# Kernel tuning notes

Hardware: AMD Instinct MI355X
Metric: run time of the kernel (lower is better)

Reference implementation:

```python
import jax, jax.numpy as jnp
import numpy as np

N = 1024      # number of nodes
D = 128       # d_x
H = 8         # num_heads


def setup_inputs() -> dict:
    key = jax.random.key(0)
    ks = jax.random.split(key, 7)
    s = (D * H) ** -0.5
    return {
        "x": jax.random.normal(ks[0], (N, D), dtype=jnp.float32),
        "spatial_encoding": jax.random.normal(ks[1], (N, N), dtype=jnp.float32),
        "edge_encoding": jax.random.normal(ks[2], (N, N), dtype=jnp.float32),
        "Wq": jax.random.normal(ks[3], (D * H, D), dtype=jnp.float32) * s,
        "Wk": jax.random.normal(ks[4], (D * H, D), dtype=jnp.float32) * s,
        "Wv": jax.random.normal(ks[5], (D * H, D), dtype=jnp.float32) * s,
        "Wo": jax.random.normal(ks[6], (D, D * H), dtype=jnp.float32) * s,
    }


def reference(x, spatial_encoding, edge_encoding, Wq, Wk, Wv, Wo):
    n, d = x.shape
    h = Wq.shape[0] // d
    scale = d ** -0.5
    # Linear (no bias), then the module's peculiar view: [n, d*h] -> [d, n, h]
    q = (x @ Wq.T).reshape(d, n, h)            # [d, n, h]
    k = (x @ Wk.T).reshape(d, n, h)            # [d, n, h]
    v = (x @ Wv.T).reshape(d, n, h)            # [d, n, h]
    # a = q @ k^T over head dim: [d, n, n]
    a = jnp.einsum('dnh,dmh->dnm', q, k) * scale
    a = a + spatial_encoding + edge_encoding   # [n,n] biases broadcast over d
    a = jax.nn.softmax(a, axis=2)
    # dropout is identity at inference
    out = jnp.einsum('dnm,dmh->dnh', a, v)     # [d, n, h]
    out = out.reshape(n, h * d)                # row-major reshape, same as torch
    return out @ Wo.T                          # [n, d]
```

## Files before the change

kernel.cpp:

```cpp
#include <hip/hip_runtime.h>
#include <hip/hip_bf16.h>
#include <math.h>

#define N_NODES 1024
#define D_DIM   128
#define H_HEADS 8
#define DH      1024

typedef short  short8 __attribute__((ext_vector_type(8)));
typedef float  f32x16 __attribute__((ext_vector_type(16)));
typedef unsigned short us4 __attribute__((ext_vector_type(4)));

static __device__ __forceinline__ unsigned short f2bf(float x) {
    __hip_bfloat16 h = __float2bfloat16(x);
    return *reinterpret_cast<unsigned short*>(&h);
}
static __device__ __forceinline__ unsigned cvt_pk_bf16(float lo, float hi) {
    unsigned r;
    asm volatile("v_cvt_pk_bf16_f32 %0, %1, %2" : "=v"(r) : "v"(lo), "v"(hi));
    return r;
}
static __device__ __forceinline__ void permlane32_swap(unsigned &a, unsigned &b) {
    asm volatile("v_permlane32_swap_b32 %0, %1" : "+v"(a), "+v"(b));
}
static __device__ __forceinline__ float fast_exp2(float x) {
    float r;
    asm("v_exp_f32 %0, %1" : "=v"(r) : "v"(x));
    return r;
}

__global__ __launch_bounds__(256) void bias_q_kernel(const float* __restrict__ sp,
                                                     const float* __restrict__ ed,
                                                     float* __restrict__ Bq) {
    __shared__ float tile[32][33];
    const int cb = blockIdx.x, rb = blockIdx.y, tid = threadIdx.x;
    const float L2E = 1.4426950408889634f;
    for (int i = tid; i < 1024; i += 256) {
        int rr = i >> 5, cc = i & 31;
        size_t g = (size_t)(rb * 32 + rr) * 1024 + cb * 32 + cc;
        tile[rr][cc] = (sp[g] + ed[g]) * L2E;
    }
    __syncthreads();
    const int c4l = tid >> 5, rr = tid & 31;
    float4 v = make_float4(tile[rr][4 * c4l + 0], tile[rr][4 * c4l + 1],
                           tile[rr][4 * c4l + 2], tile[rr][4 * c4l + 3]);
    reinterpret_cast<float4*>(Bq)[(size_t)(cb * 8 + c4l) * 1024 + rb * 32 + rr] = v;
}

__global__ __launch_bounds__(256) void qkv_mfma_kernel(const float* __restrict__ x,
                                                       const float* __restrict__ Wq,
                                                       const float* __restrict__ Wk,
                                                       const float* __restrict__ Wv,
                                                       unsigned short* __restrict__ Q,
                                                       unsigned short* __restrict__ K,
                                                       unsigned short* __restrict__ V) {
    const int tid = threadIdx.x, lane = tid & 63, wvi = tid >> 6;
    const int l31 = lane & 31, hi = lane >> 5;
    const int rb0 = blockIdx.x * 128 + wvi * 32;
    const int col = blockIdx.y * 32 + l31;
    const int m   = blockIdx.z;
    const float* W        = (m == 0) ? Wq : (m == 1) ? Wk : Wv;
    unsigned short* Out   = (m == 0) ? Q  : (m == 1) ? K  : V;
    const float osc = (m == 0) ? 0.12751879523173864f : 1.0f;

    const float* xrow = x + (size_t)(rb0 + l31) * 128 + 8 * hi;
    const float* wrow = W + (size_t)col * 128 + 8 * hi;

    f32x16 acc = {};
    #pragma unroll
    for (int ks = 0; ks < 8; ++ks) {
        float4 xa = *reinterpret_cast<const float4*>(xrow + ks * 16);
        float4 xb = *reinterpret_cast<const float4*>(xrow + ks * 16 + 4);
        float4 wa = *reinterpret_cast<const float4*>(wrow + ks * 16);
        float4 wb = *reinterpret_cast<const float4*>(wrow + ks * 16 + 4);
        union { short8 s8; unsigned u[4]; } af, bf;
        af.u[0] = cvt_pk_bf16(xa.x, xa.y); af.u[1] = cvt_pk_bf16(xa.z, xa.w);
        af.u[2] = cvt_pk_bf16(xb.x, xb.y); af.u[3] = cvt_pk_bf16(xb.z, xb.w);
        bf.u[0] = cvt_pk_bf16(wa.x, wa.y); bf.u[1] = cvt_pk_bf16(wa.z, wa.w);
        bf.u[2] = cvt_pk_bf16(wb.x, wb.y); bf.u[3] = cvt_pk_bf16(wb.z, wb.w);
        acc = __builtin_amdgcn_mfma_f32_32x32x16_bf16(af.s8, bf.s8, acc, 0, 0, 0);
    }
    #pragma unroll
    for (int i = 0; i < 16; ++i) {
        int mm = (i & 3) + 8 * (i >> 2) + 4 * hi;
        Out[(size_t)(rb0 + mm) * DH + col] = f2bf(acc[i] * osc);
    }
}

__global__ __launch_bounds__(256) void attn_kernel(const unsigned short* __restrict__ Qb,
                                                   const unsigned short* __restrict__ Kb,
                                                   const unsigned short* __restrict__ Vb,
                                                   const float* __restrict__ Bq,
                                                   unsigned short* __restrict__ Oh,
                                                   unsigned short* __restrict__ Ol) {
    __shared__ unsigned short Vt[9216];
    const int dd  = blockIdx.y;
    const int tid = threadIdx.x, lane = tid & 63, wvi = tid >> 6;
    const int l31 = lane & 31, hi = lane >> 5;

    {
        const unsigned short* src = Vb + (size_t)dd * 8192;
        char* base = reinterpret_cast<char*>(Vt);
        #pragma unroll
        for (int it = 0; it < 2; ++it) {
            int pr = it * 256 + tid;
            short8 v0 = *reinterpret_cast<const short8*>(src + (size_t)(2 * pr) * 8);
            short8 v1 = *reinterpret_cast<const short8*>(src + (size_t)(2 * pr + 1) * 8);
            #pragma unroll
            for (int h = 0; h < 8; ++h) {
                unsigned d = (unsigned)(unsigned short)v0[h] |
                             ((unsigned)(unsigned short)v1[h] << 16);
                *reinterpret_cast<unsigned*>(base + h * 2048 + ((4 * pr) ^ (h << 4))) = d;
            }
        }
        reinterpret_cast<unsigned*>(base + 16384)[tid]       = 0x3F803F80u;
        reinterpret_cast<unsigned*>(base + 16384)[tid + 256] = 0x3F803F80u;
    }
    __syncthreads();

    const int r = blockIdx.x * 128 + wvi * 32 + l31;
    short8 qf = {};
    if (!hi) qf = *reinterpret_cast<const short8*>(Qb + (size_t)dd * 8192 + (size_t)r * 8);

    f32x16 oacc = {};
    const unsigned short* kp = Kb + (size_t)dd * 8192 + (size_t)l31 * 8;
    const float4* bq4 = reinterpret_cast<const float4*>(Bq) + (size_t)hi * 1024 + r;

    auto load_bias = [&](int cbv) -> f32x16 {
        const float4* b = bq4 + (size_t)cbv * 8192;
        float4 b0 = b[0], b1 = b[2048], b2 = b[4096], b3 = b[6144];
        f32x16 o;
        o[0] = b0.x; o[1] = b0.y; o[2]  = b0.z; o[3]  = b0.w;
        o[4] = b1.x; o[5] = b1.y; o[6]  = b1.z; o[7]  = b1.w;
        o[8] = b2.x; o[9] = b2.y; o[10] = b2.z; o[11] = b2.w;
        o[12] = b3.x; o[13] = b3.y; o[14] = b3.z; o[15] = b3.w;
        return o;
    };
    auto load_k = [&](int cbv) -> short8 {
        return *reinterpret_cast<const short8*>(kp + (size_t)cbv * 256);
    };
    auto step = [&](int cbv, const f32x16& bias, const short8& kfv) {
        f32x16 sf = bias;
        sf = __builtin_amdgcn_mfma_f32_32x32x16_bf16(kfv, qf, sf, 0, 0, 0);
        float p[16];
        #pragma unroll
        for (int i = 0; i < 16; ++i) p[i] = fast_exp2(sf[i]);
        unsigned u0 = cvt_pk_bf16(p[0],  p[1]);
        unsigned u1 = cvt_pk_bf16(p[2],  p[3]);
        unsigned u2 = cvt_pk_bf16(p[4],  p[5]);
        unsigned u3 = cvt_pk_bf16(p[6],  p[7]);
        unsigned u4 = cvt_pk_bf16(p[8],  p[9]);
        unsigned u5 = cvt_pk_bf16(p[10], p[11]);
        unsigned u6 = cvt_pk_bf16(p[12], p[13]);
        unsigned u7 = cvt_pk_bf16(p[14], p[15]);
        permlane32_swap(u0, u2);
        permlane32_swap(u1, u3);
        permlane32_swap(u4, u6);
        permlane32_swap(u5, u7);
        union { short8 s8; unsigned u[4]; } pb1, pb2;
        pb1.u[0] = u0; pb1.u[1] = u1; pb1.u[2] = u2; pb1.u[3] = u3;
        pb2.u[0] = u4; pb2.u[1] = u5; pb2.u[2] = u6; pb2.u[3] = u7;

        short8 vf1 = {}, vf2 = {};
        if (l31 < 9) {
            const char* vb = reinterpret_cast<const char*>(Vt) + l31 * 2048;
            vf1 = *reinterpret_cast<const short8*>(vb + ((cbv * 64 + 16 * hi)      ^ (l31 << 4)));
            vf2 = *reinterpret_cast<const short8*>(vb + ((cbv * 64 + 32 + 16 * hi) ^ (l31 << 4)));
        }
        oacc = __builtin_amdgcn_mfma_f32_32x32x16_bf16(vf1, pb1.s8, oacc, 0, 0, 0);
        oacc = __builtin_amdgcn_mfma_f32_32x32x16_bf16(vf2, pb2.s8, oacc, 0, 0, 0);
    };

    f32x16 bA = load_bias(0), bB = load_bias(1);
    short8 kA = load_k(0),   kB = load_k(1);
    for (int cb = 0; cb < 32; cb += 2) {
        step(cb, bA, kA);
        if (cb < 30) { bA = load_bias(cb + 2); kA = load_k(cb + 2); }
        step(cb + 1, bB, kB);
        if (cb < 30) { bB = load_bias(cb + 3); kB = load_k(cb + 3); }
    }

    const float ls = oacc[4] + __shfl_xor(oacc[4], 32, 64);
    const float rl = 1.f / ls;
    us4 h4, l4;
    #pragma unroll
    for (int i = 0; i < 4; ++i) {
        float v = oacc[i] * rl;
        unsigned uv = __float_as_uint(v);
        h4[i] = (unsigned short)(uv >> 16);
        l4[i] = f2bf(v - __uint_as_float(uv & 0xFFFF0000u));
    }
    size_t off = (size_t)dd * 8192 + (size_t)r * 8 + 4 * hi;
    *reinterpret_cast<us4*>(Oh + off) = h4;
    *reinterpret_cast<us4*>(Ol + off) = l4;
}

__global__ __launch_bounds__(256) void oproj_kernel(const unsigned short* __restrict__ Oh,
                                                    const unsigned short* __restrict__ Ol,
                                                    const float* __restrict__ Wo,
                                                    float* __restrict__ out) {
    __shared__ float red[4][1024];
    const int tid = threadIdx.x, lane = tid & 63, wvi = tid >> 6;
    const int l31 = lane & 31, hi = lane >> 5;
    const int rbase = blockIdx.x * 32, cbase = blockIdx.y * 32;

    const unsigned short* ah_p = Oh + (size_t)(rbase + l31) * 1024 + wvi * 256 + 8 * hi;
    const unsigned short* al_p = Ol + (size_t)(rbase + l31) * 1024 + wvi * 256 + 8 * hi;
    const float*          b_p  = Wo + (size_t)(cbase + l31) * 1024 + wvi * 256 + 8 * hi;

    f32x16 acc = {};
    #pragma unroll
    for (int ks = 0; ks < 16; ++ks) {
        short8 ah = *reinterpret_cast<const short8*>(ah_p + ks * 16);
        short8 al = *reinterpret_cast<const short8*>(al_p + ks * 16);
        float4 w0 = *reinterpret_cast<const float4*>(b_p + ks * 16);
        float4 w1 = *reinterpret_cast<const float4*>(b_p + ks * 16 + 4);
        float w[8] = { w0.x, w0.y, w0.z, w0.w, w1.x, w1.y, w1.z, w1.w };
        union { short8 s8; unsigned u[4]; } bh, bl;
        float lo[8];
        #pragma unroll
        for (int j = 0; j < 8; ++j) {
            unsigned uv = __float_as_uint(w[j]);
            lo[j] = w[j] - __uint_as_float(uv & 0xFFFF0000u);
        }
        #pragma unroll
        for (int j = 0; j < 4; ++j) {
            unsigned e = __float_as_uint(w[2 * j]) >> 16;
            unsigned o = __float_as_uint(w[2 * j + 1]) & 0xFFFF0000u;
            bh.u[j] = e | o;
            bl.u[j] = cvt_pk_bf16(lo[2 * j], lo[2 * j + 1]);
        }
        acc = __builtin_amdgcn_mfma_f32_32x32x16_bf16(ah, bh.s8, acc, 0, 0, 0);
        acc = __builtin_amdgcn_mfma_f32_32x32x16_bf16(al, bh.s8, acc, 0, 0, 0);
        acc = __builtin_amdgcn_mfma_f32_32x32x16_bf16(ah, bl.s8, acc, 0, 0, 0);
    }
    #pragma unroll
    for (int i = 0; i < 16; ++i) {
        int mm = (i & 3) + 8 * (i >> 2) + 4 * hi;
        red[wvi][mm * 32 + l31] = acc[i];
    }
    __syncthreads();
    #pragma unroll
    for (int t = 0; t < 4; ++t) {
        int idx = tid + t * 256;
        float v = red[0][idx] + red[1][idx] + red[2][idx] + red[3][idx];
        out[(size_t)(rbase + (idx >> 5)) * D_DIM + cbase + (idx & 31)] = v;
    }
}

extern "C" void kernel_launch(void* const* d_in, const int* in_sizes, int n_in,
                              void* d_out, int out_size, void* d_ws, size_t ws_size,
                              hipStream_t stream) {
    const float* x  = (const float*)d_in[0];
    const float* sp = (const float*)d_in[1];
    const float* ed = (const float*)d_in[2];
    const float* Wq = (const float*)d_in[3];
    const float* Wk = (const float*)d_in[4];
    const float* Wv = (const float*)d_in[5];
    const float* Wo = (const float*)d_in[6];
    float* out = (float*)d_out;

    float* ws = (float*)d_ws;
    const size_t M = (size_t)N_NODES * DH;
    float* Bq = ws;
    unsigned short* Qb = (unsigned short*)(ws + M);
    unsigned short* Kb = Qb + M;
    unsigned short* Vb = Kb + M;
    unsigned short* Oh = Vb + M;
    unsigned short* Ol = Oh + M;

    bias_q_kernel<<<dim3(32, 32), 256, 0, stream>>>(sp, ed, Bq);
    qkv_mfma_kernel<<<dim3(8, 32, 3), 256, 0, stream>>>(x, Wq, Wk, Wv, Qb, Kb, Vb);
    attn_kernel<<<dim3(8, 128), 256, 0, stream>>>(Qb, Kb, Vb, Bq, Oh, Ol);
    oproj_kernel<<<dim3(32, 4), 256, 0, stream>>>(Oh, Ol, Wo, out);
}
```

Before: 68.07 us.

## Split attention keys across two chunks, merge QKV/bias prep, shrink oproj tiles

Attention now splits the key dimension into two halves, each handled by its own block, and writes unnormalized partial outputs and row sums. A new combine kernel adds the halves, normalizes, and splits the result into bf16 hi/lo. The QKV projection and bias kernels are merged into one launch. The output projection moves to 16x16 MFMA tiles to launch more blocks. The aim is more blocks and parallelism per launch; the cost is an extra kernel launch and extra fp32 partial-result traffic through memory.

New measurement: 66.42 us. 2.4% less time.

```diff
diff --git a/kernel.cpp b/kernel.cpp
--- a/kernel.cpp
+++ b/kernel.cpp
@@ -9,6 +9,7 @@
 
 typedef short  short8 __attribute__((ext_vector_type(8)));
 typedef float  f32x16 __attribute__((ext_vector_type(16)));
+typedef float  f32x4  __attribute__((ext_vector_type(4)));
 typedef unsigned short us4 __attribute__((ext_vector_type(4)));
 
 static __device__ __forceinline__ unsigned short f2bf(float x) {
@@ -29,61 +30,67 @@
     return r;
 }
 
-__global__ __launch_bounds__(256) void bias_q_kernel(const float* __restrict__ sp,
-                                                     const float* __restrict__ ed,
-                                                     float* __restrict__ Bq) {
+__global__ __launch_bounds__(256) void prep_kernel(const float* __restrict__ x,
+                                                   const float* __restrict__ Wq,
+                                                   const float* __restrict__ Wk,
+                                                   const float* __restrict__ Wv,
+                                                   const float* __restrict__ sp,
+                                                   const float* __restrict__ ed,
+                                                   unsigned short* __restrict__ Q,
+                                                   unsigned short* __restrict__ K,
+                                                   unsigned short* __restrict__ V,
+                                                   float* __restrict__ Bq) {
     __shared__ float tile[32][33];
-    const int cb = blockIdx.x, rb = blockIdx.y, tid = threadIdx.x;
-    const float L2E = 1.4426950408889634f;
-    for (int i = tid; i < 1024; i += 256) {
-        int rr = i >> 5, cc = i & 31;
-        size_t g = (size_t)(rb * 32 + rr) * 1024 + cb * 32 + cc;
-        tile[rr][cc] = (sp[g] + ed[g]) * L2E;
-    }
-    __syncthreads();
-    const int c4l = tid >> 5, rr = tid & 31;
-    float4 v = make_float4(tile[rr][4 * c4l + 0], tile[rr][4 * c4l + 1],
-                           tile[rr][4 * c4l + 2], tile[rr][4 * c4l + 3]);
-    reinterpret_cast<float4*>(Bq)[(size_t)(cb * 8 + c4l) * 1024 + rb * 32 + rr] = v;
-}
-
-__global__ __launch_bounds__(256) void qkv_mfma_kernel(const float* __restrict__ x,
-                                                       const float* __restrict__ Wq,
-                                                       const float* __restrict__ Wk,
-                                                       const float* __restrict__ Wv,
-                                                       unsigned short* __restrict__ Q,
-                                                       unsigned short* __restrict__ K,
-                                                       unsigned short* __restrict__ V) {
-    const int tid = threadIdx.x, lane = tid & 63, wvi = tid >> 6;
-    const int l31 = lane & 31, hi = lane >> 5;
-    const int rb0 = blockIdx.x * 128 + wvi * 32;
-    const int col = blockIdx.y * 32 + l31;
-    const int m   = blockIdx.z;
-    const float* W        = (m == 0) ? Wq : (m == 1) ? Wk : Wv;
-    unsigned short* Out   = (m == 0) ? Q  : (m == 1) ? K  : V;
-    const float osc = (m == 0) ? 0.12751879523173864f : 1.0f;
-
-    const float* xrow = x + (size_t)(rb0 + l31) * 128 + 8 * hi;
-    const float* wrow = W + (size_t)col * 128 + 8 * hi;
-
-    f32x16 acc = {};
-    #pragma unroll
-    for (int ks = 0; ks < 8; ++ks) {
-        float4 xa = *reinterpret_cast<const float4*>(xrow + ks * 16);
-        float4 xb = *reinterpret_cast<const float4*>(xrow + ks * 16 + 4);
-        float4 wa = *reinterpret_cast<const float4*>(wrow + ks * 16);
-        float4 wb = *reinterpret_cast<const float4*>(wrow + ks * 16 + 4);
-        union { short8 s8; unsigned u[4]; } af, bf;
-        af.u[0] = cvt_pk_bf16(xa.x, xa.y); af.u[1] = cvt_pk_bf16(xa.z, xa.w);
-        af.u[2] = cvt_pk_bf16(xb.x, xb.y); af.u[3] = cvt_pk_bf16(xb.z, xb.w);
-        bf.u[0] = cvt_pk_bf16(wa.x, wa.y); bf.u[1] = cvt_pk_bf16(wa.z, wa.w);
-        bf.u[2] = cvt_pk_bf16(wb.x, wb.y); bf.u[3] = cvt_pk_bf16(wb.z, wb.w);
-        acc = __builtin_amdgcn_mfma_f32_32x32x16_bf16(af.s8, bf.s8, acc, 0, 0, 0);
-    }
-    #pragma unroll
-    for (int i = 0; i < 16; ++i) {
-        int mm = (i & 3) + 8 * (i >> 2) + 4 * hi;
-        Out[(size_t)(rb0 + mm) * DH + col] = f2bf(acc[i] * osc);
+    const int bid = blockIdx.x;
+    const int tid = threadIdx.x;
+
+    if (bid < 768) {
+        const int lane = tid & 63, wvi = tid >> 6;
+        const int l31 = lane & 31, hi = lane >> 5;
+        const int m   = bid >> 8;
+        const int rem = bid & 255;
+        const int rb0 = (rem & 7) * 128 + wvi * 32;
+        const int col = (rem >> 3) * 32 + l31;
+        const float* W        = (m == 0) ? Wq : (m == 1) ? Wk : Wv;
+        unsigned short* Out   = (m == 0) ? Q  : (m == 1) ? K  : V;
+        const float osc = (m == 0) ? 0.12751879523173864f : 1.0f;
+
+        const float* xrow = x + (size_t)(rb0 + l31) * 128 + 8 * hi;
+        const float* wrow = W + (size_t)col * 128 + 8 * hi;
+
+        f32x16 acc = {};
+        #pragma unroll
+        for (int ks = 0; ks < 8; ++ks) {
+            float4 xa = *reinterpret_cast<const float4*>(xrow + ks * 16);
+            float4 xb = *reinterpret_cast<const float4*>(xrow + ks * 16 + 4);
+            float4 wa = *reinterpret_cast<const float4*>(wrow + ks * 16);
+            float4 wb = *reinterpret_cast<const float4*>(wrow + ks * 16 + 4);
+            union { short8 s8; unsigned u[4]; } af, bf;
+            af.u[0] = cvt_pk_bf16(xa.x, xa.y); af.u[1] = cvt_pk_bf16(xa.z, xa.w);
+            af.u[2] = cvt_pk_bf16(xb.x, xb.y); af.u[3] = cvt_pk_bf16(xb.z, xb.w);
+            bf.u[0] = cvt_pk_bf16(wa.x, wa.y); bf.u[1] = cvt_pk_bf16(wa.z, wa.w);
+            bf.u[2] = cvt_pk_bf16(wb.x, wb.y); bf.u[3] = cvt_pk_bf16(wb.z, wb.w);
+            acc = __builtin_amdgcn_mfma_f32_32x32x16_bf16(af.s8, bf.s8, acc, 0, 0, 0);
+        }
+        #pragma unroll
+        for (int i = 0; i < 16; ++i) {
+            int mm = (i & 3) + 8 * (i >> 2) + 4 * hi;
+            Out[(size_t)(rb0 + mm) * DH + col] = f2bf(acc[i] * osc);
+        }
+    } else {
+        const int b2 = bid - 768;
+        const int cb = b2 & 31, rb = b2 >> 5;
+        const float L2E = 1.4426950408889634f;
+        for (int i = tid; i < 1024; i += 256) {
+            int rr = i >> 5, cc = i & 31;
+            size_t g = (size_t)(rb * 32 + rr) * 1024 + cb * 32 + cc;
+            tile[rr][cc] = (sp[g] + ed[g]) * L2E;
+        }
+        __syncthreads();
+        const int c4l = tid >> 5, rr = tid & 31;
+        float4 v = make_float4(tile[rr][4 * c4l + 0], tile[rr][4 * c4l + 1],
+                               tile[rr][4 * c4l + 2], tile[rr][4 * c4l + 3]);
+        reinterpret_cast<float4*>(Bq)[(size_t)(cb * 8 + c4l) * 1024 + rb * 32 + rr] = v;
     }
 }
 
@@ -91,30 +98,26 @@
                                                    const unsigned short* __restrict__ Kb,
                                                    const unsigned short* __restrict__ Vb,
                                                    const float* __restrict__ Bq,
-                                                   unsigned short* __restrict__ Oh,
-                                                   unsigned short* __restrict__ Ol) {
-    __shared__ unsigned short Vt[9216];
-    const int dd  = blockIdx.y;
+                                                   float* __restrict__ Opart,
+                                                   float* __restrict__ Lpart) {
+    __shared__ unsigned short Vt[9 * 512];
+    const int dd = blockIdx.y, ch = blockIdx.z;
     const int tid = threadIdx.x, lane = tid & 63, wvi = tid >> 6;
     const int l31 = lane & 31, hi = lane >> 5;
 
     {
-        const unsigned short* src = Vb + (size_t)dd * 8192;
+        const unsigned short* src = Vb + (size_t)dd * 8192 + (size_t)ch * 4096;
         char* base = reinterpret_cast<char*>(Vt);
-        #pragma unroll
-        for (int it = 0; it < 2; ++it) {
-            int pr = it * 256 + tid;
-            short8 v0 = *reinterpret_cast<const short8*>(src + (size_t)(2 * pr) * 8);
-            short8 v1 = *reinterpret_cast<const short8*>(src + (size_t)(2 * pr + 1) * 8);
-            #pragma unroll
-            for (int h = 0; h < 8; ++h) {
-                unsigned d = (unsigned)(unsigned short)v0[h] |
-                             ((unsigned)(unsigned short)v1[h] << 16);
-                *reinterpret_cast<unsigned*>(base + h * 2048 + ((4 * pr) ^ (h << 4))) = d;
-            }
-        }
-        reinterpret_cast<unsigned*>(base + 16384)[tid]       = 0x3F803F80u;
-        reinterpret_cast<unsigned*>(base + 16384)[tid + 256] = 0x3F803F80u;
+        int pr = tid;
+        short8 v0 = *reinterpret_cast<const short8*>(src + (size_t)(2 * pr) * 8);
+        short8 v1 = *reinterpret_cast<const short8*>(src + (size_t)(2 * pr + 1) * 8);
+        #pragma unroll
+        for (int h = 0; h < 8; ++h) {
+            unsigned d = (unsigned)(unsigned short)v0[h] |
+                         ((unsigned)(unsigned short)v1[h] << 16);
+            *reinterpret_cast<unsigned*>(base + h * 1024 + ((4 * pr) ^ (h << 4))) = d;
+        }
+        reinterpret_cast<unsigned*>(base + 8 * 1024)[tid] = 0x3F803F80u;
     }
     __syncthreads();
 
@@ -123,8 +126,9 @@
     if (!hi) qf = *reinterpret_cast<const short8*>(Qb + (size_t)dd * 8192 + (size_t)r * 8);
 
     f32x16 oacc = {};
-    const unsigned short* kp = Kb + (size_t)dd * 8192 + (size_t)l31 * 8;
-    const float4* bq4 = reinterpret_cast<const float4*>(Bq) + (size_t)hi * 1024 + r;
+    const unsigned short* kp = Kb + (size_t)dd * 8192 + (size_t)(ch * 512 + l31) * 8;
+    const float4* bq4 = reinterpret_cast<const float4*>(Bq)
+                        + (size_t)ch * 131072 + (size_t)hi * 1024 + r;
 
     auto load_bias = [&](int cbv) -> f32x16 {
         const float4* b = bq4 + (size_t)cbv * 8192;
@@ -163,7 +167,7 @@
 
         short8 vf1 = {}, vf2 = {};
         if (l31 < 9) {
-            const char* vb = reinterpret_cast<const char*>(Vt) + l31 * 2048;
+            const char* vb = reinterpret_cast<const char*>(Vt) + l31 * 1024;
             vf1 = *reinterpret_cast<const short8*>(vb + ((cbv * 64 + 16 * hi)      ^ (l31 << 4)));
             vf2 = *reinterpret_cast<const short8*>(vb + ((cbv * 64 + 32 + 16 * hi) ^ (l31 << 4)));
         }
@@ -173,79 +177,84 @@
 
     f32x16 bA = load_bias(0), bB = load_bias(1);
     short8 kA = load_k(0),   kB = load_k(1);
-    for (int cb = 0; cb < 32; cb += 2) {
+    for (int cb = 0; cb < 16; cb += 2) {
         step(cb, bA, kA);
-        if (cb < 30) { bA = load_bias(cb + 2); kA = load_k(cb + 2); }
+        if (cb < 14) { bA = load_bias(cb + 2); kA = load_k(cb + 2); }
         step(cb + 1, bB, kB);
-        if (cb < 30) { bB = load_bias(cb + 3); kB = load_k(cb + 3); }
-    }
-
-    const float ls = oacc[4] + __shfl_xor(oacc[4], 32, 64);
-    const float rl = 1.f / ls;
-    us4 h4, l4;
+        if (cb < 14) { bB = load_bias(cb + 3); kB = load_k(cb + 3); }
+    }
+
+    size_t off = (size_t)ch * 1048576 + (size_t)dd * 8192 + (size_t)r * 8 + 4 * hi;
+    *reinterpret_cast<float4*>(Opart + off) =
+        make_float4(oacc[0], oacc[1], oacc[2], oacc[3]);
+    if (!hi) Lpart[(size_t)ch * 131072 + (size_t)dd * 1024 + r] = oacc[4];
+}
+
+__global__ __launch_bounds__(256) void combine_kernel(const float* __restrict__ Opart,
+                                                      const float* __restrict__ Lpart,
+                                                      unsigned short* __restrict__ Oh,
+                                                      unsigned short* __restrict__ Ol) {
+    const int gid = blockIdx.x * 256 + threadIdx.x;
+    const float4* p1 = reinterpret_cast<const float4*>(Opart) + (size_t)gid * 2;
+    const float4* p2 = reinterpret_cast<const float4*>(Opart + 1048576) + (size_t)gid * 2;
+    float4 a0 = p1[0], a1 = p1[1], b0 = p2[0], b1 = p2[1];
+    const float rl = 1.f / (Lpart[gid] + Lpart[131072 + gid]);
+    float v[8] = { (a0.x + b0.x) * rl, (a0.y + b0.y) * rl,
+                   (a0.z + b0.z) * rl, (a0.w + b0.w) * rl,
+                   (a1.x + b1.x) * rl, (a1.y + b1.y) * rl,
+                   (a1.z + b1.z) * rl, (a1.w + b1.w) * rl };
+    union { short8 s8; unsigned short us[8]; } h8, l8;
     #pragma unroll
-    for (int i = 0; i < 4; ++i) {
-        float v = oacc[i] * rl;
-        unsigned uv = __float_as_uint(v);
-        h4[i] = (unsigned short)(uv >> 16);
-        l4[i] = f2bf(v - __uint_as_float(uv & 0xFFFF0000u));
-    }
-    size_t off = (size_t)dd * 8192 + (size_t)r * 8 + 4 * hi;
-    *reinterpret_cast<us4*>(Oh + off) = h4;
-    *reinterpret_cast<us4*>(Ol + off) = l4;
+    for (int i = 0; i < 8; ++i) {
+        unsigned uv = __float_as_uint(v[i]);
+        h8.us[i] = (unsigned short)(uv >> 16);
+        l8.us[i] = f2bf(v[i] - __uint_as_float(uv & 0xFFFF0000u));
+    }
+    *reinterpret_cast<short8*>(Oh + (size_t)gid * 8) = h8.s8;
+    *reinterpret_cast<short8*>(Ol + (size_t)gid * 8) = l8.s8;
 }
 
 __global__ __launch_bounds__(256) void oproj_kernel(const unsigned short* __restrict__ Oh,
                                                     const unsigned short* __restrict__ Ol,
                                                     const float* __restrict__ Wo,
                                                     float* __restrict__ out) {
-    __shared__ float red[4][1024];
+    __shared__ float red[4][256];
     const int tid = threadIdx.x, lane = tid & 63, wvi = tid >> 6;
-    const int l31 = lane & 31, hi = lane >> 5;
-    const int rbase = blockIdx.x * 32, cbase = blockIdx.y * 32;
-
-    const unsigned short* ah_p = Oh + (size_t)(rbase + l31) * 1024 + wvi * 256 + 8 * hi;
-    const unsigned short* al_p = Ol + (size_t)(rbase + l31) * 1024 + wvi * 256 + 8 * hi;
-    const float*          b_p  = Wo + (size_t)(cbase + l31) * 1024 + wvi * 256 + 8 * hi;
-
-    f32x16 acc = {};
+    const int l15 = lane & 15, kg = lane >> 4;
+    const int rbase = blockIdx.x * 16, cbase = blockIdx.y * 16;
+
+    const unsigned short* ah_p = Oh + (size_t)(rbase + l15) * 1024 + wvi * 256 + kg * 8;
+    const unsigned short* al_p = Ol + (size_t)(rbase + l15) * 1024 + wvi * 256 + kg * 8;
+    const float*          b_p  = Wo + (size_t)(cbase + l15) * 1024 + wvi * 256 + kg * 8;
+
+    f32x4 acc = {};
     #pragma unroll
-    for (int ks = 0; ks < 16; ++ks) {
-        short8 ah = *reinterpret_cast<const short8*>(ah_p + ks * 16);
-        short8 al = *reinterpret_cast<const short8*>(al_p + ks * 16);
-        float4 w0 = *reinterpret_cast<const float4*>(b_p + ks * 16);
-        float4 w1 = *reinterpret_cast<const float4*>(b_p + ks * 16 + 4);
+    for (int ks = 0; ks < 8; ++ks) {
+        short8 ah = *reinterpret_cast<const short8*>(ah_p + ks * 32);
+        short8 al = *reinterpret_cast<const short8*>(al_p + ks * 32);
+        float4 w0 = *reinterpret_cast<const float4*>(b_p + ks * 32);
+        float4 w1 = *reinterpret_cast<const float4*>(b_p + ks * 32 + 4);
         float w[8] = { w0.x, w0.y, w0.z, w0.w, w1.x, w1.y, w1.z, w1.w };
         union { short8 s8; unsigned u[4]; } bh, bl;
-        float lo[8];
-        #pragma unroll
-        for (int j = 0; j < 8; ++j) {
-            unsigned uv = __float_as_uint(w[j]);
-            lo[j] = w[j] - __uint_as_float(uv & 0xFFFF0000u);
-        }
         #pragma unroll
         for (int j = 0; j < 4; ++j) {
             unsigned e = __float_as_uint(w[2 * j]) >> 16;
             unsigned o = __float_as_uint(w[2 * j + 1]) & 0xFFFF0000u;
             bh.u[j] = e | o;
-            bl.u[j] = cvt_pk_bf16(lo[2 * j], lo[2 * j + 1]);
-        }
-        acc = __builtin_amdgcn_mfma_f32_32x32x16_bf16(ah, bh.s8, acc, 0, 0, 0);
-        acc = __builtin_amdgcn_mfma_f32_32x32x16_bf16(al, bh.s8, acc, 0, 0, 0);
-        acc = __builtin_amdgcn_mfma_f32_32x32x16_bf16(ah, bl.s8, acc, 0, 0, 0);
+            float lo0 = w[2 * j]     - __uint_as_float(__float_as_uint(w[2 * j])     & 0xFFFF0000u);
+            float lo1 = w[2 * j + 1] - __uint_as_float(__float_as_uint(w[2 * j + 1]) & 0xFFFF0000u);
+            bl.u[j] = cvt_pk_bf16(lo0, lo1);
+        }
+        acc = __builtin_amdgcn_mfma_f32_16x16x32_bf16(ah, bh.s8, acc, 0, 0, 0);
+        acc = __builtin_amdgcn_mfma_f32_16x16x32_bf16(al, bh.s8, acc, 0, 0, 0);
+        acc = __builtin_amdgcn_mfma_f32_16x16x32_bf16(ah, bl.s8, acc, 0, 0, 0);
     }
     #pragma unroll
-    for (int i = 0; i < 16; ++i) {
-        int mm = (i & 3) + 8 * (i >> 2) + 4 * hi;
-        red[wvi][mm * 32 + l31] = acc[i];
-    }
+    for (int i = 0; i < 4; ++i)
+        red[wvi][(kg * 4 + i) * 16 + l15] = acc[i];
     __syncthreads();
-    #pragma unroll
-    for (int t = 0; t < 4; ++t) {
-        int idx = tid + t * 256;
-        float v = red[0][idx] + red[1][idx] + red[2][idx] + red[3][idx];
-        out[(size_t)(rbase + (idx >> 5)) * D_DIM + cbase + (idx & 31)] = v;
-    }
+    float v = red[0][tid & 255] + red[1][tid & 255] + red[2][tid & 255] + red[3][tid & 255];
+    out[(size_t)(rbase + (tid >> 4)) * D_DIM + cbase + (tid & 15)] = v;
 }
 
 extern "C" void kernel_launch(void* const* d_in, const int* in_sizes, int n_in,
@@ -268,9 +277,11 @@
     unsigned short* Vb = Kb + M;
     unsigned short* Oh = Vb + M;
     unsigned short* Ol = Oh + M;
-
-    bias_q_kernel<<<dim3(32, 32), 256, 0, stream>>>(sp, ed, Bq);
-    qkv_mfma_kernel<<<dim3(8, 32, 3), 256, 0, stream>>>(x, Wq, Wk, Wv, Qb, Kb, Vb);
-    attn_kernel<<<dim3(8, 128), 256, 0, stream>>>(Qb, Kb, Vb, Bq, Oh, Ol);
-    oproj_kernel<<<dim3(32, 4), 256, 0, stream>>>(Oh, Ol, Wo, out);
-}
+    float* Opart = (float*)(Ol + M);
+    float* Lpart = Opart + 2 * M;
+
+    prep_kernel<<<dim3(1792), 256, 0, stream>>>(x, Wq, Wk, Wv, sp, ed, Qb, Kb, Vb, Bq);
+    attn_kernel<<<dim3(8, 128, 2), 256, 0, stream>>>(Qb, Kb, Vb, Bq, Opart, Lpart);
+    combine_kernel<<<dim3(512), 256, 0, stream>>>(Opart, Lpart, Oh, Ol);
+    oproj_kernel<<<dim3(64, 8), 256, 0, stream>>>(Oh, Ol, Wo, out);
+}
```
